# Optimization experiments

Hardware: AMD Instinct MI355X
Metric: run time of the kernel (lower is better)

## Reference

```python
import jax, jax.numpy as jnp
import numpy as np

C = 180; NH = 6; WS = 8; SS = 4; MLP_RATIO = 2
HD = C // NH
SCALE = HD ** (-0.5)
N = WS * WS  # tokens per window


def _rel_pos_index():
    coords = np.stack(np.meshgrid(np.arange(WS), np.arange(WS), indexing='ij'))  # (2,WS,WS)
    flat = coords.reshape(2, -1)  # (2, N)
    rel = (flat[:, :, None] - flat[:, None, :]).transpose(1, 2, 0)  # (N,N,2)
    rel = rel + np.array([WS - 1, WS - 1])
    rel[:, :, 0] *= 2 * WS - 1
    return rel.sum(-1)  # (N,N) int


def _shift_mask(H, W):
    img_mask = np.zeros((H, W), dtype=np.float32)
    slices = (slice(0, -WS), slice(-WS, -SS), slice(-SS, None))
    cnt = 0
    for hs in slices:
        for ws_ in slices:
            img_mask[hs, ws_] = cnt
            cnt += 1
    mw = img_mask.reshape(H // WS, WS, W // WS, WS).transpose(0, 2, 1, 3).reshape(-1, N)  # (nW, N)
    am = mw[:, None, :] - mw[:, :, None]  # (nW, N, N)
    return np.where(am != 0, np.float32(-100.0), np.float32(0.0))


def _partition(x, H, W):
    # (B,H,W,C) -> (B*nW, N, C)
    B = x.shape[0]
    x = x.reshape(B, H // WS, WS, W // WS, WS, C).transpose(0, 1, 3, 2, 4, 5)
    return x.reshape(-1, N, C)


def _combine(w, B, H, W):
    # (B*nW, N, C) -> (B,H,W,C)
    x = w.reshape(B, H // WS, W // WS, WS, WS, C).transpose(0, 1, 3, 2, 4, 5)
    return x.reshape(B, H, W, C)


def _ln(x, g, b):
    mu = jnp.mean(x, -1, keepdims=True)
    var = jnp.mean(jnp.square(x - mu), -1, keepdims=True)
    return (x - mu) * jax.lax.rsqrt(var + 1e-5) * g + b


def setup_inputs() -> dict:
    key = jax.random.key(0)
    ks = jax.random.split(key, 10)
    B, H, W = 16, 128, 128
    s = 0.02
    return {
        'x': jax.random.normal(ks[0], (B, H * W, C), jnp.float32),
        'ln1_g': jnp.ones((C,), jnp.float32), 'ln1_b': jnp.zeros((C,), jnp.float32),
        'qkv_w': jax.random.normal(ks[1], (3 * C, C), jnp.float32) * s,
        'qkv_b': jnp.zeros((3 * C,), jnp.float32),
        'proj_w': jax.random.normal(ks[2], (C, C), jnp.float32) * s,
        'proj_b': jnp.zeros((C,), jnp.float32),
        'rpb_table': jax.random.normal(ks[3], ((2 * WS - 1) ** 2, NH), jnp.float32) * s,
        'ln2_g': jnp.ones((C,), jnp.float32), 'ln2_b': jnp.zeros((C,), jnp.float32),
        'fc1_w': jax.random.normal(ks[4], (MLP_RATIO * C, C), jnp.float32) * s,
        'fc1_b': jnp.zeros((MLP_RATIO * C,), jnp.float32),
        'fc2_w': jax.random.normal(ks[5], (C, MLP_RATIO * C), jnp.float32) * s,
        'fc2_b': jnp.zeros((C,), jnp.float32),
        'img_height': 128, 'img_width': 128,
    }


def reference(x, ln1_g, ln1_b, qkv_w, qkv_b, proj_w, proj_b, rpb_table,
              ln2_g, ln2_b, fc1_w, fc1_b, fc2_w, fc2_b, img_height, img_width):
    H, W = int(img_height), int(img_width)
    B = x.shape[0]
    rpi = jnp.asarray(_rel_pos_index().reshape(-1))           # (N*N,) static
    mask = jnp.asarray(_shift_mask(H, W))                     # (nW, N, N) static
    nW = (H // WS) * (W // WS)

    residual = x
    h = _ln(x, ln1_g, ln1_b).reshape(B, H, W, C)
    h = jnp.roll(h, (-SS, -SS), axis=(1, 2))
    xw = _partition(h, H, W)                                  # (B*nW, N, C)

    qkv = xw @ qkv_w.T + qkv_b                                # (B*nW, N, 3C)
    qkv = qkv.reshape(-1, N, 3, NH, HD).transpose(2, 0, 3, 1, 4)
    q, k, v = qkv[0] * SCALE, qkv[1], qkv[2]                  # (B*nW, NH, N, HD)
    scores = jnp.einsum('whnd,whmd->whnm', q, k)              # (B*nW, NH, N, N)
    bias = rpb_table[rpi].reshape(N, N, NH).transpose(2, 0, 1)  # (NH,N,N)
    scores = scores + bias[None]
    scores = scores.reshape(B, nW, NH, N, N) + mask[None, :, None]
    probs = jax.nn.softmax(scores.reshape(-1, NH, N, N), axis=-1)
    out = jnp.einsum('whnm,whmd->whnd', probs, v)             # (B*nW, NH, N, HD)
    out = out.transpose(0, 2, 1, 3).reshape(-1, N, C)
    out = out @ proj_w.T + proj_b

    h = _combine(out, B, H, W)
    h = jnp.roll(h, (SS, SS), axis=(1, 2)).reshape(B, H * W, C)
    h = h + residual
    m = _ln(h, ln2_g, ln2_b)
    m = jax.nn.gelu(m @ fc1_w.T + fc1_b, approximate=False) @ fc2_w.T + fc2_b
    return h + m
```

## Files before the change

kernel.cpp:

```cpp
#include <hip/hip_runtime.h>
#include <hip/hip_bf16.h>

typedef short s16x8 __attribute__((ext_vector_type(8)));
typedef short s16x4 __attribute__((ext_vector_type(4)));
typedef float f32x4 __attribute__((ext_vector_type(4)));

__device__ __forceinline__ short f2bf(float f) {
    __bf16 h = (__bf16)f;
    return __builtin_bit_cast(short, h);
}
__device__ __forceinline__ float bf2f(short s) {
    return __builtin_bit_cast(float, ((unsigned int)(unsigned short)s) << 16);
}
__device__ __forceinline__ unsigned int pk2(float a, float b) {
    return (unsigned int)(unsigned short)f2bf(a) | ((unsigned int)(unsigned short)f2bf(b) << 16);
}
__device__ __forceinline__ f32x4 mfma16(s16x8 a, s16x8 b, f32x4 c) {
    return __builtin_amdgcn_mfma_f32_16x16x32_bf16(a, b, c, 0, 0, 0);
}
__device__ __forceinline__ s16x8 ld_b64x2(const short* p) {
    union { s16x8 v; s16x4 h[2]; } u;
    u.h[0] = *(const s16x4*)p;
    u.h[1] = *(const s16x4*)(p + 4);
    return u.v;
}
__device__ __forceinline__ s16x4 pack4(f32x4 a) {
    s16x4 w;
    w[0] = f2bf(a[0]); w[1] = f2bf(a[1]); w[2] = f2bf(a[2]); w[3] = f2bf(a[3]);
    return w;
}

#define SCALE_Q 0.18257418583505536f
#define ONE_BF16 ((short)0x3F80)
#define RA 204
#define PS 76
#define HS 196


__global__ void k_prep(const float* __restrict__ qkv_w, const float* __restrict__ qkv_b,
                       const float* __restrict__ proj_w, const float* __restrict__ proj_b,
                       const float* __restrict__ fc1_w, const float* __restrict__ fc1_b,
                       const float* __restrict__ fc2_w,
                       const float* __restrict__ rpb,
                       short* __restrict__ Whead, short* __restrict__ Wproj,
                       short* __restrict__ Wfc1, short* __restrict__ Wfc2,
                       short* __restrict__ battn) {
    int gt = blockIdx.x * 256 + threadIdx.x;
    int stride = gridDim.x * 256;
    for (int idx = gt; idx < 6 * 96 * 192; idx += stride) {
        int h = idx / (96 * 192), rem = idx - h * 96 * 192;
        int rr = rem / 192, kk = rem - rr * 192;
        int seg = rr >> 5, hd = rr & 31;
        float val = 0.f;
        if (hd < 30) {
            int ch = seg * 180 + h * 30 + hd;
            if (kk < 180) val = qkv_w[ch * 180 + kk];
            else if (kk == 180) val = qkv_b[ch];
            if (seg == 0) val *= SCALE_Q;
        }
        Whead[idx] = f2bf(val);
    }
    for (int idx = gt; idx < 192 * 192; idx += stride) {
        int rr = idx / 192, kk = idx - rr * 192;
        float val = 0.f;
        if (rr < 180) {
            if (kk < 180) val = proj_w[rr * 180 + kk];
            else if (kk == 180) val = proj_b[rr];
        }
        Wproj[idx] = f2bf(val);
    }
    for (int idx = gt; idx < 384 * 192; idx += stride) {
        int rr = idx / 192, kk = idx - rr * 192;
        float val = 0.f;
        if (rr < 360) {
            if (kk < 180) val = fc1_w[rr * 180 + kk];
            else if (kk == 180) val = fc1_b[rr];
        }
        Wfc1[idx] = f2bf(val);
    }
    for (int idx = gt; idx < 192 * 384; idx += stride) {
        int rr = idx / 384, kk = idx - rr * 384;
        Wfc2[idx] = (rr < 180 && kk < 360) ? f2bf(fc2_w[rr * 360 + kk]) : (short)0;
    }
    for (int idx = gt; idx < 6 * 64 * 64; idx += stride) {
        int h = idx >> 12, n = (idx >> 6) & 63, m = idx & 63;
        int r1 = n >> 3, c1 = n & 7, r2 = m >> 3, c2 = m & 7;
        int ridx = (r1 - r2 + 7) * 15 + (c1 - c2 + 7);
        battn[idx] = f2bf(rpb[ridx * 6 + h]);
    }
}

__global__ __launch_bounds__(768, 3)
void k_fused(const float* __restrict__ x, const float* __restrict__ g1, const float* __restrict__ b1,
             const short* __restrict__ Whead,
             const short* __restrict__ Wproj,
             const short* __restrict__ battn,
             const float* __restrict__ g2, const float* __restrict__ b2,
             const short* __restrict__ Wfc1,
             const short* __restrict__ Wfc2, const float* __restrict__ fb2,
             float* __restrict__ out) {
    __shared__ __align__(16) char smem[160768];

    const int tid = threadIdx.x;
    const int wvg = tid >> 6;
    const int half = (wvg >= 6) ? 1 : 0;
    const int wv = wvg - half * 6;
    const int l = tid & 63, l15 = l & 15, lg = l >> 4;
    const int tl = tid - half * 384;

    char* sm = smem + half * 80384;
    short* xln  = (short*)sm;
    short* xout = (short*)sm;
    short* ylds = (short*)sm;
    short* mo   = (short*)sm;
    short* regP = (short*)(sm + 26112);
    short* pout = regP;
    short* ybuf = regP;
    short* hid  = (short*)(sm + 55296);
    short* patch = regP + wv * 2432;

    const int wid = blockIdx.x * 2 + half;
    const int b = wid >> 8, win = wid & 255, wi = win >> 4, wj = win & 15;
    const bool edge = (wi == 15) || (wj == 15);
    const f32x4 vzero = {0.f, 0.f, 0.f, 0.f};

    const int t = tl >> 2, sub = tl & 3;
    size_t rowbase = 0;
    if (tl < 256) {
        const int r = t >> 3, c = t & 7;
        const int gi = (wi * 8 + r + 4) & 127, gj = (wj * 8 + c + 4) & 127;
        rowbase = ((size_t)b * 16384 + (size_t)gi * 128 + gj) * 180;
    }
    const float* xrow = x + rowbase;
    float* yrow = out + rowbase;

    float4 xr[12];

    if (tl < 256) {
        float s1 = 0.f, s2 = 0.f;
#pragma unroll
        for (int m = 0; m < 12; ++m) {
            int jj = sub + 4 * m;
            if (jj < 45) {
                float4 t4 = *(const float4*)&xrow[4 * jj];
                xr[m] = t4;
                s1 += t4.x + t4.y + t4.z + t4.w;
                s2 += t4.x * t4.x + t4.y * t4.y + t4.z * t4.z + t4.w * t4.w;
            }
        }
        s1 += __shfl_xor(s1, 1); s2 += __shfl_xor(s2, 1);
        s1 += __shfl_xor(s1, 2); s2 += __shfl_xor(s2, 2);
        const float mu = s1 * (1.f / 180.f);
        const float rstd = rsqrtf(s2 * (1.f / 180.f) - mu * mu + 1e-5f);
#pragma unroll
        for (int m = 0; m < 12; ++m) {
            int jj = sub + 4 * m;
            if (jj < 45) {
                float4 g4 = *(const float4*)&g1[4 * jj];
                float4 b4 = *(const float4*)&b1[4 * jj];
                s16x4 w;
                w[0] = f2bf((xr[m].x - mu) * rstd * g4.x + b4.x);
                w[1] = f2bf((xr[m].y - mu) * rstd * g4.y + b4.y);
                w[2] = f2bf((xr[m].z - mu) * rstd * g4.z + b4.z);
                w[3] = f2bf((xr[m].w - mu) * rstd * g4.w + b4.w);
                *(s16x4*)&xln[t * RA + 4 * jj] = w;
            }
        }
    } else {
        for (int k = tl - 256; k < 64 * 12; k += 128) {
            int rr = k / 12, cc = k - rr * 12;
            xln[rr * RA + 180 + cc] = (cc == 0) ? ONE_BF16 : (short)0;
        }
    }
    __syncthreads();

    const short* Wh = Whead + wv * (96 * 192);
    s16x8 qf[4], kf[4], vf[2][2];

#pragma unroll
    for (int jl = 0; jl < 2; ++jl) {
        f32x4 acc[4] = {vzero, vzero, vzero, vzero};
#pragma unroll
        for (int ks = 0; ks < 6; ++ks) {
            s16x8 bwk = *(const s16x8*)&Wh[(jl * 16 + l15) * 192 + ks * 32 + lg * 8];
#pragma unroll
            for (int i = 0; i < 4; ++i) {
                s16x8 afi = ld_b64x2(&xln[(i * 16 + l15) * RA + ks * 32 + lg * 8]);
                acc[i] = mfma16(bwk, afi, acc[i]);
            }
        }
#pragma unroll
        for (int i = 0; i < 4; ++i)
            *(s16x4*)&patch[(i * 16 + l15) * 36 + jl * 16 + lg * 4] = pack4(acc[i]);
    }
#pragma unroll
    for (int i = 0; i < 4; ++i) qf[i] = ld_b64x2(&patch[(i * 16 + l15) * 36 + lg * 8]);

#pragma unroll
    for (int jl = 0; jl < 2; ++jl) {
        f32x4 acc[4] = {vzero, vzero, vzero, vzero};
#pragma unroll
        for (int ks = 0; ks < 6; ++ks) {
            s16x8 bwk = *(const s16x8*)&Wh[(32 + jl * 16 + l15) * 192 + ks * 32 + lg * 8];
#pragma unroll
            for (int i = 0; i < 4; ++i) {
                s16x8 afi = ld_b64x2(&xln[(i * 16 + l15) * RA + ks * 32 + lg * 8]);
                acc[i] = mfma16(bwk, afi, acc[i]);
            }
        }
#pragma unroll
        for (int i = 0; i < 4; ++i)
            *(s16x4*)&patch[(i * 16 + l15) * 36 + jl * 16 + lg * 4] = pack4(acc[i]);
    }
#pragma unroll
    for (int j = 0; j < 4; ++j) kf[j] = ld_b64x2(&patch[(j * 16 + l15) * 36 + lg * 8]);

#pragma unroll
    for (int jl = 0; jl < 2; ++jl) {
        f32x4 acc[4] = {vzero, vzero, vzero, vzero};
#pragma unroll
        for (int ks = 0; ks < 6; ++ks) {
            s16x8 bwk = *(const s16x8*)&Wh[(64 + jl * 16 + l15) * 192 + ks * 32 + lg * 8];
#pragma unroll
            for (int i = 0; i < 4; ++i) {
                s16x8 afi = ld_b64x2(&xln[(i * 16 + l15) * RA + ks * 32 + lg * 8]);
                acc[i] = mfma16(afi, bwk, acc[i]);
            }
        }
#pragma unroll
        for (int i = 0; i < 4; ++i)
            *(s16x4*)&patch[(jl * 16 + l15) * PS + i * 16 + lg * 4] = pack4(acc[i]);
    }
#pragma unroll
    for (int j2 = 0; j2 < 2; ++j2)
#pragma unroll
        for (int ksv = 0; ksv < 2; ++ksv)
            vf[j2][ksv] = ld_b64x2(&patch[(j2 * 16 + l15) * PS + ksv * 32 + lg * 8]);

    __syncthreads();

    {
        const short* bb = battn + wv * 4096;
#pragma unroll
        for (int i = 0; i < 4; ++i) {
            const int n = i * 16 + l15;
            f32x4 sc[4];
#pragma unroll
            for (int j = 0; j < 4; ++j) sc[j] = mfma16(kf[j], qf[i], vzero);
            int cnt_n = 0;
            if (edge) {
                int rn = n >> 3, cn = n & 7;
                cnt_n = (wi == 15 ? ((rn >= 4) ? 2 : 1) : 0) * 3 + (wj == 15 ? ((cn >= 4) ? 2 : 1) : 0);
            }
            float p[4][4];
#pragma unroll
            for (int j = 0; j < 4; ++j) {
                s16x4 bv = *(const s16x4*)&bb[n * 64 + j * 16 + lg * 4];
#pragma unroll
                for (int tt = 0; tt < 4; ++tt) {
                    float s = sc[j][tt] + bf2f(bv[tt]);
                    if (edge) {
                        int m = j * 16 + lg * 4 + tt;
                        int rm = m >> 3, cm = m & 7;
                        int cnt_m = (wi == 15 ? ((rm >= 4) ? 2 : 1) : 0) * 3 + (wj == 15 ? ((cm >= 4) ? 2 : 1) : 0);
                        if (cnt_m != cnt_n) s -= 100.f;
                    }
                    p[j][tt] = s;
                }
            }
            float m0 = p[0][0];
#pragma unroll
            for (int j = 0; j < 4; ++j)
#pragma unroll
                for (int tt = 0; tt < 4; ++tt) m0 = fmaxf(m0, p[j][tt]);
            m0 = fmaxf(m0, __shfl_xor(m0, 16));
            m0 = fmaxf(m0, __shfl_xor(m0, 32));
            float s0 = 0.f;
#pragma unroll
            for (int j = 0; j < 4; ++j)
#pragma unroll
                for (int tt = 0; tt < 4; ++tt) { float e = __expf(p[j][tt] - m0); p[j][tt] = e; s0 += e; }
            s0 += __shfl_xor(s0, 16);
            s0 += __shfl_xor(s0, 32);
            const float sm0 = __builtin_amdgcn_rcpf(s0);

            short* pb = patch + (i & 1) * 1216;
#pragma unroll
            for (int j = 0; j < 4; ++j) {
                f32x4 ps;
#pragma unroll
                for (int tt = 0; tt < 4; ++tt) ps[tt] = p[j][tt] * sm0;
                *(s16x4*)&pb[l15 * PS + j * 16 + lg * 4] = pack4(ps);
            }
            s16x8 pa0 = ld_b64x2(&pb[l15 * PS + lg * 8]);
            s16x8 pa1 = ld_b64x2(&pb[l15 * PS + 32 + lg * 8]);
            f32x4 ov0 = mfma16(vf[0][0], pa0, vzero);
            ov0 = mfma16(vf[0][1], pa1, ov0);
            f32x4 ov1 = mfma16(vf[1][0], pa0, vzero);
            ov1 = mfma16(vf[1][1], pa1, ov1);
            short* xo = &xout[n * RA + wv * 30];
            unsigned int w0 = pk2(ov0[0], ov0[1]);
            unsigned int w1 = pk2(ov0[2], ov0[3]);
            *(unsigned int*)&xo[lg * 4] = w0;
            *(unsigned int*)&xo[lg * 4 + 2] = w1;
            unsigned int w2 = pk2(ov1[0], ov1[1]);
            if (lg < 3) {
                unsigned int w3 = pk2(ov1[2], ov1[3]);
                *(unsigned int*)&xo[16 + lg * 4] = w2;
                *(unsigned int*)&xo[16 + lg * 4 + 2] = w3;
            } else {
                *(unsigned int*)&xo[28] = w2;
            }
        }
    }
    __syncthreads();

#pragma unroll
    for (int jl = 0; jl < 2; ++jl) {
        const int cb = wv * 32 + jl * 16 + lg * 4;
        f32x4 acc[4] = {vzero, vzero, vzero, vzero};
#pragma unroll
        for (int ks = 0; ks < 6; ++ks) {
            s16x8 bwk = *(const s16x8*)&Wproj[(wv * 32 + jl * 16 + l15) * 192 + ks * 32 + lg * 8];
#pragma unroll
            for (int i = 0; i < 4; ++i) {
                s16x8 afi = ld_b64x2(&xout[(i * 16 + l15) * RA + ks * 32 + lg * 8]);
                acc[i] = mfma16(bwk, afi, acc[i]);
            }
        }
        if (cb <= 176) {
#pragma unroll
            for (int i = 0; i < 4; ++i)
                *(s16x4*)&pout[(i * 16 + l15) * RA + cb] = pack4(acc[i]);
        }
    }
    __syncthreads();

    if (tl < 256) {
        float s1 = 0.f, s2 = 0.f;
        unsigned int pA[12], pB[12];
#pragma unroll
        for (int m = 0; m < 12; ++m) {
            int jj = sub + 4 * m;
            if (jj < 45) {
                s16x4 pv = *(const s16x4*)&pout[t * RA + 4 * jj];
                float4 y4;
                y4.x = xr[m].x + bf2f(pv[0]); y4.y = xr[m].y + bf2f(pv[1]);
                y4.z = xr[m].z + bf2f(pv[2]); y4.w = xr[m].w + bf2f(pv[3]);
                pA[m] = pk2(y4.x, y4.y);
                pB[m] = pk2(y4.z, y4.w);
                *(unsigned int*)&ybuf[t * RA + 4 * jj] = pA[m];
                *(unsigned int*)&ybuf[t * RA + 4 * jj + 2] = pB[m];
                s1 += y4.x + y4.y + y4.z + y4.w;
                s2 += y4.x * y4.x + y4.y * y4.y + y4.z * y4.z + y4.w * y4.w;
            }
        }
        s1 += __shfl_xor(s1, 1); s2 += __shfl_xor(s2, 1);
        s1 += __shfl_xor(s1, 2); s2 += __shfl_xor(s2, 2);
        const float mu = s1 * (1.f / 180.f);
        const float rstd = rsqrtf(s2 * (1.f / 180.f) - mu * mu + 1e-5f);
#pragma unroll
        for (int m = 0; m < 12; ++m) {
            int jj = sub + 4 * m;
            if (jj < 45) {
                float4 g4 = *(const float4*)&g2[4 * jj];
                float4 b4 = *(const float4*)&b2[4 * jj];
                float ylo0 = bf2f((short)(pA[m] & 0xFFFFu));
                float yhi0 = bf2f((short)(pA[m] >> 16));
                float ylo1 = bf2f((short)(pB[m] & 0xFFFFu));
                float yhi1 = bf2f((short)(pB[m] >> 16));
                s16x4 w;
                w[0] = f2bf((ylo0 - mu) * rstd * g4.x + b4.x);
                w[1] = f2bf((yhi0 - mu) * rstd * g4.y + b4.y);
                w[2] = f2bf((ylo1 - mu) * rstd * g4.z + b4.z);
                w[3] = f2bf((yhi1 - mu) * rstd * g4.w + b4.w);
                *(s16x4*)&ylds[t * RA + 4 * jj] = w;
            }
        }
    } else {
        for (int k = tl - 256; k < 64 * 12; k += 128) {
            int rr = k / 12, cc = k - rr * 12;
            ylds[rr * RA + 180 + cc] = (cc == 0) ? ONE_BF16 : (short)0;
        }
    }
    __syncthreads();

    f32x4 acc3[2][4];
#pragma unroll
    for (int jl = 0; jl < 2; ++jl)
#pragma unroll
        for (int i = 0; i < 4; ++i) acc3[jl][i] = vzero;

#pragma unroll
    for (int kh = 0; kh < 2; ++kh) {
#pragma unroll
        for (int jl = 0; jl < 2; ++jl) {
            f32x4 acc[4] = {vzero, vzero, vzero, vzero};
#pragma unroll
            for (int ks = 0; ks < 6; ++ks) {
                s16x8 bwk = *(const s16x8*)&Wfc1[((kh * 12 + wv * 2 + jl) * 16 + l15) * 192 + ks * 32 + lg * 8];
#pragma unroll
                for (int i = 0; i < 4; ++i) {
                    s16x8 ai = ld_b64x2(&ylds[(i * 16 + l15) * RA + ks * 32 + lg * 8]);
                    acc[i] = mfma16(bwk, ai, acc[i]);
                }
            }
            const int clb = (wv * 2 + jl) * 16 + lg * 4;
#pragma unroll
            for (int i = 0; i < 4; ++i) {
                s16x4 w;
#pragma unroll
                for (int tt = 0; tt < 4; ++tt) {
                    float v = acc[i][tt];
                    float u = v * (1.f + 0.044715f * v * v);
                    float e = __expf(-1.5957691216f * u);
                    w[tt] = f2bf(v * __builtin_amdgcn_rcpf(1.f + e));
                }
                *(s16x4*)&hid[(i * 16 + l15) * HS + clb] = w;
            }
        }
        __syncthreads();
#pragma unroll
        for (int ks = 0; ks < 6; ++ks) {
            s16x8 a[4];
#pragma unroll
            for (int i = 0; i < 4; ++i)
                a[i] = ld_b64x2(&hid[(i * 16 + l15) * HS + ks * 32 + lg * 8]);
#pragma unroll
            for (int jl = 0; jl < 2; ++jl) {
                s16x8 bw2 = *(const s16x8*)&Wfc2[((wv * 2 + jl) * 16 + l15) * 384 + kh * 192 + ks * 32 + lg * 8];
#pragma unroll
                for (int i = 0; i < 4; ++i) acc3[jl][i] = mfma16(bw2, a[i], acc3[jl][i]);
            }
        }
        __syncthreads();
    }

#pragma unroll
    for (int jl = 0; jl < 2; ++jl) {
        const int cb = (wv * 2 + jl) * 16 + lg * 4;
        if (cb <= 176) {
            float4 f4 = *(const float4*)&fb2[cb];
#pragma unroll
            for (int i = 0; i < 4; ++i) {
                f32x4 a2;
                a2[0] = acc3[jl][i][0] + f4.x;
                a2[1] = acc3[jl][i][1] + f4.y;
                a2[2] = acc3[jl][i][2] + f4.z;
                a2[3] = acc3[jl][i][3] + f4.w;
                *(s16x4*)&mo[(i * 16 + l15) * RA + cb] = pack4(a2);
            }
        }
    }
    __syncthreads();

    if (tl < 256) {
#pragma unroll
        for (int m = 0; m < 12; ++m) {
            int jj = sub + 4 * m;
            if (jj < 45) {
                s16x4 yv4 = *(const s16x4*)&ybuf[t * RA + 4 * jj];
                s16x4 mv = *(const s16x4*)&mo[t * RA + 4 * jj];
                float4 o;
                o.x = bf2f(yv4[0]) + bf2f(mv[0]);
                o.y = bf2f(yv4[1]) + bf2f(mv[1]);
                o.z = bf2f(yv4[2]) + bf2f(mv[2]);
                o.w = bf2f(yv4[3]) + bf2f(mv[3]);
                *(float4*)&yrow[4 * jj] = o;
            }
        }
    }
}

extern "C" void kernel_launch(void* const* d_in, const int* in_sizes, int n_in,
                              void* d_out, int out_size, void* d_ws, size_t ws_size,
                              hipStream_t stream) {
    (void)in_sizes; (void)n_in; (void)out_size; (void)ws_size;
    const float* x      = (const float*)d_in[0];
    const float* ln1g   = (const float*)d_in[1];
    const float* ln1b   = (const float*)d_in[2];
    const float* qkv_w  = (const float*)d_in[3];
    const float* qkv_b  = (const float*)d_in[4];
    const float* proj_w = (const float*)d_in[5];
    const float* proj_b = (const float*)d_in[6];
    const float* rpb    = (const float*)d_in[7];
    const float* ln2g   = (const float*)d_in[8];
    const float* ln2b   = (const float*)d_in[9];
    const float* fc1_w  = (const float*)d_in[10];
    const float* fc1_b  = (const float*)d_in[11];
    const float* fc2_w  = (const float*)d_in[12];
    const float* fc2_b  = (const float*)d_in[13];
    float* out = (float*)d_out;

    char* ws = (char*)d_ws;
    short* Whead = (short*)(ws + 0);
    short* Wproj = (short*)(ws + 221184);
    short* Wfc1  = (short*)(ws + 294912);
    short* Wfc2  = (short*)(ws + 442368);
    short* battn = (short*)(ws + 589824);

    k_prep<<<256, 256, 0, stream>>>(qkv_w, qkv_b, proj_w, proj_b, fc1_w, fc1_b, fc2_w, rpb,
                                    Whead, Wproj, Wfc1, Wfc2, battn);
    k_fused<<<2048, 768, 0, stream>>>(x, ln1g, ln1b, Whead, Wproj, battn,
                                      ln2g, ln2b, Wfc1, Wfc2, fc2_b, out);
}
```

Baseline: 467.7 us.

## Remap LDS regions to drop a barrier and add MFMA priority hints

Rearranges the shared-memory layout so xout/ybuf live in a separate region from the QKV patch buffers. This lets the barrier between the QKV projection and attention be removed, and the hidden buffer now reuses the patch region. Wave 0 now writes the padding columns of xout. MFMA loops are wrapped in s_setprio raise/lower hints, and the LN2 path keeps the fp32 residual sum instead of re-reading the bf16-rounded copy. The aim is fewer block-wide stalls and better interleaving of waves, at the cost of a little more LDS, which could reduce occupancy.

```diff
diff --git a/kernel.cpp b/kernel.cpp
--- a/kernel.cpp
+++ b/kernel.cpp
@@ -35,6 +35,8 @@
 #define RA 204
 #define PS 76
 #define HS 196
+#define PRIO_HI() __builtin_amdgcn_s_setprio(1)
+#define PRIO_LO() __builtin_amdgcn_s_setprio(0)
 
 
 __global__ void k_prep(const float* __restrict__ qkv_w, const float* __restrict__ qkv_b,
@@ -99,7 +101,7 @@
              const short* __restrict__ Wfc1,
              const short* __restrict__ Wfc2, const float* __restrict__ fb2,
              float* __restrict__ out) {
-    __shared__ __align__(16) char smem[160768];
+    __shared__ __align__(16) char smem[162816];
 
     const int tid = threadIdx.x;
     const int wvg = tid >> 6;
@@ -108,16 +110,17 @@
     const int l = tid & 63, l15 = l & 15, lg = l >> 4;
     const int tl = tid - half * 384;
 
-    char* sm = smem + half * 80384;
+    char* sm = smem + half * 81408;
     short* xln  = (short*)sm;
-    short* xout = (short*)sm;
     short* ylds = (short*)sm;
     short* mo   = (short*)sm;
     short* regP = (short*)(sm + 26112);
     short* pout = regP;
-    short* ybuf = regP;
-    short* hid  = (short*)(sm + 55296);
+    short* hid  = regP;
     short* patch = regP + wv * 2432;
+    short* regX = (short*)(sm + 55296);
+    short* xout = regX;
+    short* ybuf = regX;
 
     const int wid = blockIdx.x * 2 + half;
     const int b = wid >> 8, win = wid & 255, wi = win >> 4, wj = win & 15;
@@ -180,6 +183,7 @@
 #pragma unroll
     for (int jl = 0; jl < 2; ++jl) {
         f32x4 acc[4] = {vzero, vzero, vzero, vzero};
+        PRIO_HI();
 #pragma unroll
         for (int ks = 0; ks < 6; ++ks) {
             s16x8 bwk = *(const s16x8*)&Wh[(jl * 16 + l15) * 192 + ks * 32 + lg * 8];
@@ -189,6 +193,7 @@
                 acc[i] = mfma16(bwk, afi, acc[i]);
             }
         }
+        PRIO_LO();
 #pragma unroll
         for (int i = 0; i < 4; ++i)
             *(s16x4*)&patch[(i * 16 + l15) * 36 + jl * 16 + lg * 4] = pack4(acc[i]);
@@ -199,6 +204,7 @@
 #pragma unroll
     for (int jl = 0; jl < 2; ++jl) {
         f32x4 acc[4] = {vzero, vzero, vzero, vzero};
+        PRIO_HI();
 #pragma unroll
         for (int ks = 0; ks < 6; ++ks) {
             s16x8 bwk = *(const s16x8*)&Wh[(32 + jl * 16 + l15) * 192 + ks * 32 + lg * 8];
@@ -208,6 +214,7 @@
                 acc[i] = mfma16(bwk, afi, acc[i]);
             }
         }
+        PRIO_LO();
 #pragma unroll
         for (int i = 0; i < 4; ++i)
             *(s16x4*)&patch[(i * 16 + l15) * 36 + jl * 16 + lg * 4] = pack4(acc[i]);
@@ -218,6 +225,7 @@
 #pragma unroll
     for (int jl = 0; jl < 2; ++jl) {
         f32x4 acc[4] = {vzero, vzero, vzero, vzero};
+        PRIO_HI();
 #pragma unroll
         for (int ks = 0; ks < 6; ++ks) {
             s16x8 bwk = *(const s16x8*)&Wh[(64 + jl * 16 + l15) * 192 + ks * 32 + lg * 8];
@@ -227,6 +235,7 @@
                 acc[i] = mfma16(afi, bwk, acc[i]);
             }
         }
+        PRIO_LO();
 #pragma unroll
         for (int i = 0; i < 4; ++i)
             *(s16x4*)&patch[(jl * 16 + l15) * PS + i * 16 + lg * 4] = pack4(acc[i]);
@@ -237,7 +246,6 @@
         for (int ksv = 0; ksv < 2; ++ksv)
             vf[j2][ksv] = ld_b64x2(&patch[(j2 * 16 + l15) * PS + ksv * 32 + lg * 8]);
 
-    __syncthreads();
 
     {
         const short* bb = battn + wv * 4096;
@@ -245,8 +253,10 @@
         for (int i = 0; i < 4; ++i) {
             const int n = i * 16 + l15;
             f32x4 sc[4];
+            PRIO_HI();
 #pragma unroll
             for (int j = 0; j < 4; ++j) sc[j] = mfma16(kf[j], qf[i], vzero);
+            PRIO_LO();
             int cnt_n = 0;
             if (edge) {
                 int rn = n >> 3, cn = n & 7;
@@ -294,10 +304,12 @@
             }
             s16x8 pa0 = ld_b64x2(&pb[l15 * PS + lg * 8]);
             s16x8 pa1 = ld_b64x2(&pb[l15 * PS + 32 + lg * 8]);
+            PRIO_HI();
             f32x4 ov0 = mfma16(vf[0][0], pa0, vzero);
             ov0 = mfma16(vf[0][1], pa1, ov0);
             f32x4 ov1 = mfma16(vf[1][0], pa0, vzero);
             ov1 = mfma16(vf[1][1], pa1, ov1);
+            PRIO_LO();
             short* xo = &xout[n * RA + wv * 30];
             unsigned int w0 = pk2(ov0[0], ov0[1]);
             unsigned int w1 = pk2(ov0[2], ov0[3]);
@@ -313,12 +325,19 @@
             }
         }
     }
+    if (wv == 0) {
+        for (int k = l; k < 64 * 12; k += 64) {
+            int rr = k / 12, cc = k - rr * 12;
+            xout[rr * RA + 180 + cc] = (cc == 0) ? ONE_BF16 : (short)0;
+        }
+    }
     __syncthreads();
 
 #pragma unroll
     for (int jl = 0; jl < 2; ++jl) {
         const int cb = wv * 32 + jl * 16 + lg * 4;
         f32x4 acc[4] = {vzero, vzero, vzero, vzero};
+        PRIO_HI();
 #pragma unroll
         for (int ks = 0; ks < 6; ++ks) {
             s16x8 bwk = *(const s16x8*)&Wproj[(wv * 32 + jl * 16 + l15) * 192 + ks * 32 + lg * 8];
@@ -328,6 +347,7 @@
                 acc[i] = mfma16(bwk, afi, acc[i]);
             }
         }
+        PRIO_LO();
         if (cb <= 176) {
 #pragma unroll
             for (int i = 0; i < 4; ++i)
@@ -338,7 +358,7 @@
 
     if (tl < 256) {
         float s1 = 0.f, s2 = 0.f;
-        unsigned int pA[12], pB[12];
+        float4 yv[12];
 #pragma unroll
         for (int m = 0; m < 12; ++m) {
             int jj = sub + 4 * m;
@@ -347,10 +367,9 @@
                 float4 y4;
                 y4.x = xr[m].x + bf2f(pv[0]); y4.y = xr[m].y + bf2f(pv[1]);
                 y4.z = xr[m].z + bf2f(pv[2]); y4.w = xr[m].w + bf2f(pv[3]);
-                pA[m] = pk2(y4.x, y4.y);
-                pB[m] = pk2(y4.z, y4.w);
-                *(unsigned int*)&ybuf[t * RA + 4 * jj] = pA[m];
-                *(unsigned int*)&ybuf[t * RA + 4 * jj + 2] = pB[m];
+                yv[m] = y4;
+                *(unsigned int*)&ybuf[t * RA + 4 * jj] = pk2(y4.x, y4.y);
+                *(unsigned int*)&ybuf[t * RA + 4 * jj + 2] = pk2(y4.z, y4.w);
                 s1 += y4.x + y4.y + y4.z + y4.w;
                 s2 += y4.x * y4.x + y4.y * y4.y + y4.z * y4.z + y4.w * y4.w;
             }
@@ -365,15 +384,11 @@
             if (jj < 45) {
                 float4 g4 = *(const float4*)&g2[4 * jj];
                 float4 b4 = *(const float4*)&b2[4 * jj];
-                float ylo0 = bf2f((short)(pA[m] & 0xFFFFu));
-                float yhi0 = bf2f((short)(pA[m] >> 16));
-                float ylo1 = bf2f((short)(pB[m] & 0xFFFFu));
-                float yhi1 = bf2f((short)(pB[m] >> 16));
                 s16x4 w;
-                w[0] = f2bf((ylo0 - mu) * rstd * g4.x + b4.x);
-                w[1] = f2bf((yhi0 - mu) * rstd * g4.y + b4.y);
-                w[2] = f2bf((ylo1 - mu) * rstd * g4.z + b4.z);
-                w[3] = f2bf((yhi1 - mu) * rstd * g4.w + b4.w);
+                w[0] = f2bf((yv[m].x - mu) * rstd * g4.x + b4.x);
+                w[1] = f2bf((yv[m].y - mu) * rstd * g4.y + b4.y);
+                w[2] = f2bf((yv[m].z - mu) * rstd * g4.z + b4.z);
+                w[3] = f2bf((yv[m].w - mu) * rstd * g4.w + b4.w);
                 *(s16x4*)&ylds[t * RA + 4 * jj] = w;
             }
         }
@@ -396,6 +411,7 @@
 #pragma unroll
         for (int jl = 0; jl < 2; ++jl) {
             f32x4 acc[4] = {vzero, vzero, vzero, vzero};
+            PRIO_HI();
 #pragma unroll
             for (int ks = 0; ks < 6; ++ks) {
                 s16x8 bwk = *(const s16x8*)&Wfc1[((kh * 12 + wv * 2 + jl) * 16 + l15) * 192 + ks * 32 + lg * 8];
@@ -405,6 +421,7 @@
                     acc[i] = mfma16(bwk, ai, acc[i]);
                 }
             }
+            PRIO_LO();
             const int clb = (wv * 2 + jl) * 16 + lg * 4;
 #pragma unroll
             for (int i = 0; i < 4; ++i) {
@@ -420,6 +437,7 @@
             }
         }
         __syncthreads();
+        PRIO_HI();
 #pragma unroll
         for (int ks = 0; ks < 6; ++ks) {
             s16x8 a[4];
@@ -433,6 +451,7 @@
                 for (int i = 0; i < 4; ++i) acc3[jl][i] = mfma16(bw2, a[i], acc3[jl][i]);
             }
         }
+        PRIO_LO();
         __syncthreads();
     }
 
```

After: 496.1 us. 1.06x slower.
